# Kernel tuning notes

Hardware: AMD Instinct MI355X
Metric: run time of the kernel (lower is better)

Reference implementation:

```python
import jax, jax.numpy as jnp
import numpy as np
from jax import lax

EPS = 1e-5


def setup_inputs() -> dict:
    key = jax.random.key(0)
    ks = jax.random.split(key, 8)
    B, N, dim = 16, 2048, 128
    x = jax.random.normal(ks[0], (B, 3, N), dtype=jnp.float32)
    W1 = jax.random.normal(ks[1], (dim, 3), dtype=jnp.float32) * 0.1
    W2 = jax.random.normal(ks[2], (dim, dim), dtype=jnp.float32) * 0.05
    W3 = jax.random.normal(ks[3], (dim, dim), dtype=jnp.float32) * 0.05
    zeros = jnp.zeros((dim,), jnp.float32)
    ones = jnp.ones((dim,), jnp.float32)
    return {
        "x": x,
        "W1": W1, "b1": zeros, "g1": ones, "be1": zeros,
        "W2": W2, "b2": zeros, "g2": ones, "be2": zeros,
        "W3": W3, "b3": zeros, "g3": ones, "be3": zeros,
        "k": 8,
    }


def _bn_relu(y, g, be):
    # training-mode batch norm over (B, k, N) per channel, then ReLU
    m = jnp.mean(y, axis=(0, 2, 3), keepdims=True)
    v = jnp.var(y, axis=(0, 2, 3), keepdims=True)
    yhat = (y - m) * lax.rsqrt(v + EPS)
    return jax.nn.relu(yhat * g[None, :, None, None] + be[None, :, None, None])


def _group(x, k):
    # x: [B, 3, N] -> relative kNN offsets [B, 3, k, N] (DGCNN-style, self included)
    sq = jnp.sum(x * x, axis=1)                       # [B, N]
    inner = jnp.einsum('bcn,bcm->bnm', x, x)          # [B, N, N]
    dist = sq[:, :, None] - 2.0 * inner + sq[:, None, :]
    _, idx = lax.top_k(-dist, k)                      # [B, N, k] nearest neighbors
    gathered = jax.vmap(lambda xb, ib: xb[:, ib])(x, idx)  # [B, 3, N, k]
    grouped = gathered - x[:, :, :, None]             # subtract center point
    return jnp.transpose(grouped, (0, 1, 3, 2))       # [B, 3, k, N]


def reference(x, W1, b1, g1, be1, W2, b2, g2, be2, W3, b3, g3, be3, k):
    out = _group(x, k)                                          # [B, 3, k, N]
    h = jnp.einsum('bckn,dc->bdkn', out, W1) + b1[None, :, None, None]
    h = _bn_relu(h, g1, be1)
    h = jnp.einsum('bckn,dc->bdkn', h, W2) + b2[None, :, None, None]
    h = _bn_relu(h, g2, be2)
    h = jnp.einsum('bckn,dc->bdkn', h, W3) + b3[None, :, None, None]
    h = _bn_relu(h, g3, be3)
    return jnp.max(h, axis=2)                                   # [B, dim, N]
```

## Files before the change

### kernel.cpp

```cpp
#include <hip/hip_runtime.h>
#include <hip/hip_bf16.h>
#include <math.h>


#define B_   16
#define N_   2048
#define KNN  8
#define DIM  128
#define P_   (B_*N_*KNN)
#define CAP  128
#define NBLK 2048

typedef __attribute__((ext_vector_type(8))) short bf16x8;
typedef __attribute__((ext_vector_type(4))) short bf16x4;
typedef __attribute__((ext_vector_type(4))) float f32x4;

#define OFF_G     0ull
#define SZ_G      ((size_t)3*P_*4)
#define OFF_Y2B   (OFF_G + SZ_G)
#define SZ_Y2B    ((size_t)DIM*P_*2)
#define OFF_STATS (OFF_Y2B + SZ_Y2B)
#define N_STATS   4112
#define SZ_STATS  ((size_t)N_STATS*8)
#define OFF_AB    (OFF_STATS + SZ_STATS)
#define SZ_AB     4096ull
#define OFF_KPART (OFF_AB + SZ_AB)
#define NKBLK     2048
#define SZ_KPART  ((size_t)9*NKBLK*4)
#define OFF_YMM   (OFF_KPART + SZ_KPART)
#define SZ_YMM    ((size_t)DIM*NBLK*16*4)

#define I_S2   16
#define I_S3   (16 + 8*256)
#define NBANK  8

#define AB_W1F 0
#define AB_A2  512
#define AB_E2  640
#define AB_A3  768
#define AB_E3  896

#define DPP_XOR1   0xB1
#define DPP_XOR2   0x4E
#define DPP_HALFM  0x141
#define DPP_MIRROR 0x140

template<int C>
__device__ __forceinline__ float dppf(float v) {
    return __int_as_float(__builtin_amdgcn_update_dpp(
        __float_as_int(v), __float_as_int(v), C, 0xF, 0xF, false));
}

__device__ __forceinline__ void atomAddD(double* p, double v) {
    __hip_atomic_fetch_add(p, v, __ATOMIC_RELAXED, __HIP_MEMORY_SCOPE_AGENT);
}
__device__ __forceinline__ unsigned short f2bs(float f) {
    const unsigned b = __float_as_uint(f);
    return (unsigned short)((b + 0x7FFFu + ((b >> 16) & 1u)) >> 16);
}
__device__ __forceinline__ float bs2f(unsigned short u) {
    return __uint_as_float(((unsigned)u) << 16);
}

__global__ __launch_bounds__(1024) void knn_group_kernel(
    const float* __restrict__ x, float* __restrict__ g,
    float* __restrict__ kpart, double* __restrict__ st)
{
    __shared__ __align__(16) float4 xs4[N_];
    __shared__ unsigned long long listK[16][CAP];
    __shared__ float spart[16][12];
    const int b   = blockIdx.y;
    const int tid = threadIdx.x;
    const int wv  = tid >> 6;
    const int ln  = tid & 63;
    const int n   = blockIdx.x * 16 + wv;
    const float* xb = x + (size_t)b * 3 * N_;

    if (blockIdx.x == 0 && blockIdx.y == 0)
        for (int i = tid; i < N_STATS; i += 1024) st[i] = 0.0;

    for (int i = tid; i < N_; i += 1024) {
        const float a0 = xb[i], a1 = xb[N_ + i], a2 = xb[2*N_ + i];
        const float sq = __fadd_rn(__fadd_rn(__fmul_rn(a0,a0), __fmul_rn(a1,a1)), __fmul_rn(a2,a2));
        xs4[i] = make_float4(a0, a1, a2, sq);
    }
    __syncthreads();

    const float4 me = xs4[n];
    const float xn0 = me.x, xn1 = me.y, xn2 = me.z, sqn = me.w;

    float dreg[32];
    float lmin = INFINITY;
    #pragma unroll
    for (int i = 0; i < 32; ++i) {
        const float4 q = xs4[ln + 64*i];
        dreg[i] = __fadd_rn(__fmaf_rn(-2.f, __fmaf_rn(xn2, q.z, __fmaf_rn(xn1, q.y, __fmul_rn(xn0, q.x))), sqn), q.w);
        lmin = fminf(lmin, dreg[i]);
    }

    float gm = lmin;
    gm = fminf(gm, __shfl_xor(gm, 1));
    gm = fminf(gm, __shfl_xor(gm, 2));
    gm = fminf(gm, __shfl_xor(gm, 4));
    float Bb = gm;
    Bb = fmaxf(Bb, __shfl_xor(Bb, 8));
    Bb = fmaxf(Bb, __shfl_xor(Bb, 16));
    Bb = fmaxf(Bb, __shfl_xor(Bb, 32));

    unsigned base = 0;
    #pragma unroll
    for (int i = 0; i < 32; ++i) {
        const bool pred = (dreg[i] <= Bb);
        const unsigned long long mk = __ballot(pred);
        if (pred) {
            const unsigned pos = base + (unsigned)__popcll(mk & ((1ull << ln) - 1ull));
            if (pos < CAP) {
                const unsigned u = __float_as_uint(dreg[i]);
                const unsigned od = u ^ ((unsigned)(((int)u) >> 31) | 0x80000000u);
                listK[wv][pos] = (((unsigned long long)od) << 32) | (unsigned)(ln + 64*i);
            }
        }
        base += (unsigned)__popcll(mk);
    }
    const int cnt = (base < CAP) ? (int)base : CAP;

    int myi = 0;
    if (cnt <= 64) {
        unsigned long long K = (ln < cnt) ? listK[wv][ln] : ~0ull;
        #pragma unroll
        for (int k = 2; k <= 64; k <<= 1) {
            #pragma unroll
            for (int j = k >> 1; j >= 1; j >>= 1) {
                const unsigned long long o = __shfl_xor(K, j);
                const bool takeMin = (((ln & j) == 0) == ((ln & k) == 0));
                const bool oLess = (o < K);
                if (takeMin ? oLess : !oLess) K = o;
            }
        }
        myi = (int)(unsigned)K;
    } else {
        unsigned long long K0 = (ln < cnt)      ? listK[wv][ln]      : ~0ull;
        unsigned long long K1 = (ln + 64 < cnt) ? listK[wv][ln + 64] : ~0ull;
        #pragma unroll
        for (int sel = 0; sel < 8; ++sel) {
            unsigned long long p = (K1 < K0) ? K1 : K0;
            #pragma unroll
            for (int m = 1; m < 64; m <<= 1) {
                const unsigned long long o = __shfl_xor(p, m);
                if (o < p) p = o;
            }
            if (ln == sel) myi = (int)(unsigned)p;
            if (K0 == p) K0 = ~0ull;
            if (K1 == p) K1 = ~0ull;
        }
    }

    if (ln < 8) {
        const float4 q = xs4[myi];
        const float g0  = q.x - xn0;
        const float g1v = q.y - xn1;
        const float g2v = q.z - xn2;
        const size_t basep = ((size_t)b*N_ + n) * KNN;
        g[0*P_ + basep + ln] = g0;
        g[1*P_ + basep + ln] = g1v;
        g[2*P_ + basep + ln] = g2v;
        float s0 = g0, s1 = g1v, s2 = g2v;
        float s00 = g0*g0, s01 = g0*g1v, s02 = g0*g2v;
        float s11 = g1v*g1v, s12 = g1v*g2v, s22 = g2v*g2v;
        #pragma unroll
        for (int m = 1; m < 8; m <<= 1) {
            s0 += __shfl_xor(s0, m);  s1 += __shfl_xor(s1, m);  s2 += __shfl_xor(s2, m);
            s00 += __shfl_xor(s00, m); s01 += __shfl_xor(s01, m); s02 += __shfl_xor(s02, m);
            s11 += __shfl_xor(s11, m); s12 += __shfl_xor(s12, m); s22 += __shfl_xor(s22, m);
        }
        if (ln == 0) {
            spart[wv][0] = s0;  spart[wv][1] = s1;  spart[wv][2] = s2;
            spart[wv][3] = s00; spart[wv][4] = s01; spart[wv][5] = s02;
            spart[wv][6] = s11; spart[wv][7] = s12; spart[wv][8] = s22;
        }
    }
    __syncthreads();
    if (tid < 9) {
        float a = 0.f;
        #pragma unroll
        for (int w = 0; w < 16; ++w) a += spart[w][tid];
        kpart[tid*NKBLK + blockIdx.y*128 + blockIdx.x] = a;
    }
}

__global__ __launch_bounds__(1024) void finalize1_kernel(
    const float* __restrict__ kpart, const float* __restrict__ W1,
    const float* __restrict__ b1, const float* __restrict__ g1,
    const float* __restrict__ be1, float* __restrict__ ab)
{
    __shared__ double S9[9];
    const int tid = threadIdx.x;
    const int w = tid >> 6, l = tid & 63;
    if (w < 9) {
        double a = 0.0;
        #pragma unroll
        for (int i = 0; i < 32; ++i) a += (double)kpart[w*NKBLK + l + 64*i];
        #pragma unroll
        for (int m = 1; m < 64; m <<= 1) a += __shfl_xor(a, m);
        if (l == 0) S9[w] = a;
    }
    __syncthreads();
    if (tid < 128) {
        const int d = tid;
        const double inv = 1.0 / (double)P_;
        const double mu0 = S9[0]*inv, mu1 = S9[1]*inv, mu2 = S9[2]*inv;
        const double c00 = S9[3]*inv - mu0*mu0;
        const double c01 = S9[4]*inv - mu0*mu1;
        const double c02 = S9[5]*inv - mu0*mu2;
        const double c11 = S9[6]*inv - mu1*mu1;
        const double c12 = S9[7]*inv - mu1*mu2;
        const double c22 = S9[8]*inv - mu2*mu2;
        const double w0 = W1[d*3+0], w1 = W1[d*3+1], w2 = W1[d*3+2];
        const double mean = w0*mu0 + w1*mu1 + w2*mu2 + (double)b1[d];
        double var = w0*w0*c00 + w1*w1*c11 + w2*w2*c22
                   + 2.0*(w0*w1*c01 + w0*w2*c02 + w1*w2*c12);
        if (var < 0.0) var = 0.0;
        const double r = 1.0 / sqrt(var + 1e-5);
        const double alpha = (double)g1[d] * r;
        const double beta  = (double)be1[d] - mean*alpha;
        ab[AB_W1F + 4*d + 0] = (float)(alpha * w0);
        ab[AB_W1F + 4*d + 1] = (float)(alpha * w1);
        ab[AB_W1F + 4*d + 2] = (float)(alpha * w2);
        ab[AB_W1F + 4*d + 3] = (float)(alpha * (double)b1[d] + beta);
    }
}

__global__ void finalize23_kernel(
    const double* __restrict__ st, int soff,
    const float* __restrict__ gg, const float* __restrict__ bee,
    float* __restrict__ ab, int aoff)
{
    const int d = threadIdx.x;
    if (d >= DIM) return;
    double s1 = 0.0, s2 = 0.0;
    #pragma unroll
    for (int k = 0; k < NBANK; ++k) {
        s1 += st[soff + k*256 + d];
        s2 += st[soff + k*256 + 128 + d];
    }
    const double inv = 1.0 / (double)P_;
    const double mean = s1 * inv;
    double var = s2 * inv - mean*mean;
    if (var < 0.0) var = 0.0;
    const double r = 1.0 / sqrt(var + 1e-5);
    const double alpha = (double)gg[d] * r;
    ab[aoff + d]       = (float)alpha;
    ab[aoff + 128 + d] = (float)((double)bee[d] - mean*alpha);
}

template<int SRC, int MODE>
__global__ __launch_bounds__(512) void conv_kernel(
    const float* __restrict__ gsrc, const unsigned short* __restrict__ ybsrc,
    const float* __restrict__ Wf, const float* __restrict__ ab,
    const float* __restrict__ bias, unsigned short* __restrict__ ybdst,
    unsigned* __restrict__ ymm, double* __restrict__ stats, int statoff)
{
    __shared__ __align__(16) short Hs[128*136];
    const int tid = threadIdx.x;
    const int p0g = blockIdx.x * 128;
    const int w  = tid >> 6;
    const int ln = tid & 63;
    const int lg = ln >> 4, lr = ln & 15;

    bf16x8 afrag[4];
    #pragma unroll
    for (int ks = 0; ks < 4; ++ks) {
        const float* wr = &Wf[(size_t)(16*w + lr)*DIM + (4*ks + lg)*8];
        const float4 a4 = *(const float4*)wr;
        const float4 b4 = *(const float4*)(wr + 4);
        bf16x8 f;
        f[0]=(short)f2bs(a4.x); f[1]=(short)f2bs(a4.y); f[2]=(short)f2bs(a4.z); f[3]=(short)f2bs(a4.w);
        f[4]=(short)f2bs(b4.x); f[5]=(short)f2bs(b4.y); f[6]=(short)f2bs(b4.z); f[7]=(short)f2bs(b4.w);
        afrag[ks] = f;
    }

    if constexpr (SRC == 0) {
        const int sp = tid & 127;
        const int ob = tid >> 7;
        const float gx = gsrc[0*P_ + p0g + sp];
        const float gy = gsrc[1*P_ + p0g + sp];
        const float gz = gsrc[2*P_ + p0g + sp];
        #pragma unroll
        for (int it = 0; it < 4; ++it) {
            const int o = ob + 4*it;
            bf16x8 hv;
            #pragma unroll
            for (int j = 0; j < 8; ++j) {
                const int c = 8*o + j;
                const float4 wf = *(const float4*)&ab[AB_W1F + 4*c];
                const float h = fmaxf(__fmaf_rn(wf.x, gx, __fmaf_rn(wf.y, gy, __fmaf_rn(wf.z, gz, wf.w))), 0.f);
                hv[j] = (short)f2bs(h);
            }
            *(bf16x8*)&Hs[sp*128 + ((o ^ (sp & 7)) * 8)] = hv;
        }
    } else {
        const int myoct = tid & 15;
        const float4 aLo = *(const float4*)&ab[AB_A2 + myoct*8];
        const float4 aHi = *(const float4*)&ab[AB_A2 + myoct*8 + 4];
        const float4 eLo = *(const float4*)&ab[AB_E2 + myoct*8];
        const float4 eHi = *(const float4*)&ab[AB_E2 + myoct*8 + 4];
        const float av[8] = {aLo.x,aLo.y,aLo.z,aLo.w,aHi.x,aHi.y,aHi.z,aHi.w};
        const float ev[8] = {eLo.x,eLo.y,eLo.z,eLo.w,eHi.x,eHi.y,eHi.z,eHi.w};
        #pragma unroll
        for (int it = 0; it < 4; ++it) {
            const int p = it*32 + (tid >> 4);
            const bf16x8 raw = *(const bf16x8*)&ybsrc[(size_t)(p0g + p)*128 + myoct*8];
            bf16x8 hv;
            #pragma unroll
            for (int j = 0; j < 8; ++j) {
                const float v = bs2f((unsigned short)raw[j]);
                hv[j] = (short)f2bs(fmaxf(__fmaf_rn(av[j], v, ev[j]), 0.f));
            }
            *(bf16x8*)&Hs[p*128 + ((myoct ^ (p & 7)) * 8)] = hv;
        }
    }
    __syncthreads();

    f32x4 acc[8];
    #pragma unroll
    for (int j = 0; j < 8; ++j) acc[j] = (f32x4){0.f, 0.f, 0.f, 0.f};

    #pragma unroll
    for (int ks = 0; ks < 4; ++ks) {
        #pragma unroll
        for (int pt = 0; pt < 8; ++pt) {
            const int p = 16*pt + lr;
            const bf16x8 bf = *(const bf16x8*)&Hs[p*128 + (((4*ks + lg) ^ (lr & 7)) * 8)];
            acc[pt] = __builtin_amdgcn_mfma_f32_16x16x32_bf16(afrag[ks], bf, acc[pt], 0, 0, 0);
        }
    }

    const int bank = blockIdx.x & (NBANK-1);
    #pragma unroll
    for (int r = 0; r < 4; ++r) {
        const int d = 16*w + 4*lg + r;
        const float bb = bias[d];
        float v[8];
        #pragma unroll
        for (int pt = 0; pt < 8; ++pt) v[pt] = acc[pt][r] + bb;

        float s1 = ((v[0]+v[1])+(v[2]+v[3])) + ((v[4]+v[5])+(v[6]+v[7]));
        float s2 = ((v[0]*v[0]+v[1]*v[1])+(v[2]*v[2]+v[3]*v[3]))
                 + ((v[4]*v[4]+v[5]*v[5])+(v[6]*v[6]+v[7]*v[7]));
        s1 += dppf<DPP_XOR1>(s1);  s2 += dppf<DPP_XOR1>(s2);
        s1 += dppf<DPP_XOR2>(s1);  s2 += dppf<DPP_XOR2>(s2);
        s1 += dppf<DPP_HALFM>(s1); s2 += dppf<DPP_HALFM>(s2);
        s1 += dppf<DPP_MIRROR>(s1); s2 += dppf<DPP_MIRROR>(s2);
        if (lr == 0) {
            atomAddD(&stats[statoff + bank*256 + d], (double)s1);
            atomAddD(&stats[statoff + bank*256 + 128 + d], (double)s2);
        }

        if constexpr (MODE == 3) {
            #pragma unroll
            for (int pt = 0; pt < 8; ++pt) {
                float mx = v[pt], mn = v[pt];
                mx = fmaxf(mx, dppf<DPP_XOR1>(mx));  mn = fminf(mn, dppf<DPP_XOR1>(mn));
                mx = fmaxf(mx, dppf<DPP_XOR2>(mx));  mn = fminf(mn, dppf<DPP_XOR2>(mn));
                mx = fmaxf(mx, dppf<DPP_HALFM>(mx)); mn = fminf(mn, dppf<DPP_HALFM>(mn));
                if ((lr & 7) == 0) {
                    const int slot = 2*pt + (lr >> 3);
                    ymm[((size_t)d*NBLK + blockIdx.x)*16 + slot] =
                        (unsigned)f2bs(mx) | ((unsigned)f2bs(mn) << 16);
                }
            }
        }
    }

    if constexpr (MODE == 0) {
        __syncthreads();
        const int d0 = 16*w + 4*lg;
        const float4 b4 = *(const float4*)&bias[d0];
        #pragma unroll
        for (int pt = 0; pt < 8; ++pt) {
            const int p = 16*pt + lr;
            bf16x4 pk;
            pk[0] = (short)f2bs(acc[pt][0] + b4.x);
            pk[1] = (short)f2bs(acc[pt][1] + b4.y);
            pk[2] = (short)f2bs(acc[pt][2] + b4.z);
            pk[3] = (short)f2bs(acc[pt][3] + b4.w);
            *(bf16x4*)&Hs[p*136 + d0] = pk;
        }
        __syncthreads();
        #pragma unroll
        for (int it = 0; it < 4; ++it) {
            const int f = it*512 + tid;
            const int row = f >> 4, ch = f & 15;
            const bf16x8 vv = *(const bf16x8*)&Hs[row*136 + ch*8];
            *(bf16x8*)&ybdst[(size_t)(p0g + row)*128 + ch*8] = vv;
        }
    }
}

__global__ __launch_bounds__(256) void bn3max_kernel(
    const unsigned* __restrict__ ymm, const float* __restrict__ ab, float* __restrict__ out)
{
    const int idx = blockIdx.x*256 + threadIdx.x;
    const int n = idx & (N_-1);
    const int d = (idx >> 11) & (DIM-1);
    const int b = idx >> 18;
    const int pt  = b*N_ + n;
    const int blk = pt >> 4;
    const int j   = pt & 15;
    const unsigned pk = ymm[((size_t)d*NBLK + blk)*16 + j];
    const float a = ab[AB_A3 + d], e = ab[AB_E3 + d];
    const float mx = bs2f((unsigned short)(pk & 0xFFFF));
    const float mn = bs2f((unsigned short)(pk >> 16));
    const float v = (a >= 0.f) ? mx : mn;
    out[idx] = fmaxf(__fmaf_rn(a, v, e), 0.f);
}

extern "C" void kernel_launch(void* const* d_in, const int* in_sizes, int n_in,
                              void* d_out, int out_size, void* d_ws, size_t ws_size,
                              hipStream_t stream) {
    (void)in_sizes; (void)n_in; (void)out_size; (void)ws_size;
    const float* x   = (const float*)d_in[0];
    const float* W1  = (const float*)d_in[1];
    const float* b1  = (const float*)d_in[2];
    const float* g1  = (const float*)d_in[3];
    const float* be1 = (const float*)d_in[4];
    const float* W2  = (const float*)d_in[5];
    const float* b2  = (const float*)d_in[6];
    const float* g2  = (const float*)d_in[7];
    const float* be2 = (const float*)d_in[8];
    const float* W3  = (const float*)d_in[9];
    const float* b3  = (const float*)d_in[10];
    const float* g3  = (const float*)d_in[11];
    const float* be3 = (const float*)d_in[12];

    float*  out = (float*)d_out;
    char*   ws  = (char*)d_ws;
    float*          g   = (float*)(ws + OFF_G);
    unsigned short* y2t = (unsigned short*)(ws + OFF_Y2B);
    double*         st  = (double*)(ws + OFF_STATS);
    float*          ab  = (float*)(ws + OFF_AB);
    float*          kp  = (float*)(ws + OFF_KPART);
    unsigned*       ymm = (unsigned*)(ws + OFF_YMM);

    knn_group_kernel<<<dim3(128, B_), 1024, 0, stream>>>(x, g, kp, st);
    finalize1_kernel<<<1, 1024, 0, stream>>>(kp, W1, b1, g1, be1, ab);
    conv_kernel<0,0><<<NBLK, 512, 0, stream>>>(g, nullptr, W2, ab, b2, y2t, nullptr, st, I_S2);
    finalize23_kernel<<<1, 128, 0, stream>>>(st, I_S2, g2, be2, ab, AB_A2);
    conv_kernel<1,3><<<NBLK, 512, 0, stream>>>(nullptr, y2t, W3, ab, b3, nullptr, ymm, st, I_S3);
    finalize23_kernel<<<1, 128, 0, stream>>>(st, I_S3, g3, be3, ab, AB_A3);
    bn3max_kernel<<<(B_*DIM*N_)/256, 256, 0, stream>>>(ymm, ab, out);
}
```

Before: 153.5 us.

## Fold BN finalize kernels into consumers and process two points per kNN wave

Removes the two single-block finalize23 launches by having each conv_kernel<1,3> block and each bn3max block recompute the per-channel BN affine from the double stats into shared memory. Also makes each kNN wave handle two query points, halving the grid and reusing each shared-memory point load for two distance rows. This trades two launches and their serial gaps for redundant stats reads in every block (many blocks in bn3max), and doubles distance registers per thread in the kNN kernel, which may lower occupancy.

```diff
diff --git a/kernel.cpp b/kernel.cpp
--- a/kernel.cpp
+++ b/kernel.cpp
@@ -10,6 +10,7 @@
 #define P_   (B_*N_*KNN)
 #define CAP  128
 #define NBLK 2048
+#define KBLKS 1024
 
 typedef __attribute__((ext_vector_type(8))) short bf16x8;
 typedef __attribute__((ext_vector_type(4))) short bf16x4;
@@ -25,8 +26,7 @@
 #define OFF_AB    (OFF_STATS + SZ_STATS)
 #define SZ_AB     4096ull
 #define OFF_KPART (OFF_AB + SZ_AB)
-#define NKBLK     2048
-#define SZ_KPART  ((size_t)9*NKBLK*4)
+#define SZ_KPART  ((size_t)9*2048*4)
 #define OFF_YMM   (OFF_KPART + SZ_KPART)
 #define SZ_YMM    ((size_t)DIM*NBLK*16*4)
 
@@ -35,10 +35,6 @@
 #define NBANK  8
 
 #define AB_W1F 0
-#define AB_A2  512
-#define AB_E2  640
-#define AB_A3  768
-#define AB_E3  896
 
 #define DPP_XOR1   0xB1
 #define DPP_XOR2   0x4E
@@ -62,42 +58,10 @@
     return __uint_as_float(((unsigned)u) << 16);
 }
 
-__global__ __launch_bounds__(1024) void knn_group_kernel(
-    const float* __restrict__ x, float* __restrict__ g,
-    float* __restrict__ kpart, double* __restrict__ st)
-{
-    __shared__ __align__(16) float4 xs4[N_];
-    __shared__ unsigned long long listK[16][CAP];
-    __shared__ float spart[16][12];
-    const int b   = blockIdx.y;
-    const int tid = threadIdx.x;
-    const int wv  = tid >> 6;
-    const int ln  = tid & 63;
-    const int n   = blockIdx.x * 16 + wv;
-    const float* xb = x + (size_t)b * 3 * N_;
-
-    if (blockIdx.x == 0 && blockIdx.y == 0)
-        for (int i = tid; i < N_STATS; i += 1024) st[i] = 0.0;
-
-    for (int i = tid; i < N_; i += 1024) {
-        const float a0 = xb[i], a1 = xb[N_ + i], a2 = xb[2*N_ + i];
-        const float sq = __fadd_rn(__fadd_rn(__fmul_rn(a0,a0), __fmul_rn(a1,a1)), __fmul_rn(a2,a2));
-        xs4[i] = make_float4(a0, a1, a2, sq);
-    }
-    __syncthreads();
-
-    const float4 me = xs4[n];
-    const float xn0 = me.x, xn1 = me.y, xn2 = me.z, sqn = me.w;
-
-    float dreg[32];
-    float lmin = INFINITY;
-    #pragma unroll
-    for (int i = 0; i < 32; ++i) {
-        const float4 q = xs4[ln + 64*i];
-        dreg[i] = __fadd_rn(__fmaf_rn(-2.f, __fmaf_rn(xn2, q.z, __fmaf_rn(xn1, q.y, __fmul_rn(xn0, q.x))), sqn), q.w);
-        lmin = fminf(lmin, dreg[i]);
-    }
-
+__device__ __forceinline__ int select8(
+    const float (&dreg)[32], float lmin,
+    unsigned long long* __restrict__ listKw, int ln)
+{
     float gm = lmin;
     gm = fminf(gm, __shfl_xor(gm, 1));
     gm = fminf(gm, __shfl_xor(gm, 2));
@@ -117,7 +81,7 @@
             if (pos < CAP) {
                 const unsigned u = __float_as_uint(dreg[i]);
                 const unsigned od = u ^ ((unsigned)(((int)u) >> 31) | 0x80000000u);
-                listK[wv][pos] = (((unsigned long long)od) << 32) | (unsigned)(ln + 64*i);
+                listKw[pos] = (((unsigned long long)od) << 32) | (unsigned)(ln + 64*i);
             }
         }
         base += (unsigned)__popcll(mk);
@@ -126,7 +90,7 @@
 
     int myi = 0;
     if (cnt <= 64) {
-        unsigned long long K = (ln < cnt) ? listK[wv][ln] : ~0ull;
+        unsigned long long K = (ln < cnt) ? listKw[ln] : ~0ull;
         #pragma unroll
         for (int k = 2; k <= 64; k <<= 1) {
             #pragma unroll
@@ -139,8 +103,8 @@
         }
         myi = (int)(unsigned)K;
     } else {
-        unsigned long long K0 = (ln < cnt)      ? listK[wv][ln]      : ~0ull;
-        unsigned long long K1 = (ln + 64 < cnt) ? listK[wv][ln + 64] : ~0ull;
+        unsigned long long K0 = (ln < cnt)      ? listKw[ln]      : ~0ull;
+        unsigned long long K1 = (ln + 64 < cnt) ? listKw[ln + 64] : ~0ull;
         #pragma unroll
         for (int sel = 0; sel < 8; ++sel) {
             unsigned long long p = (K1 < K0) ? K1 : K0;
@@ -154,19 +118,88 @@
             if (K1 == p) K1 = ~0ull;
         }
     }
+    return myi;
+}
+
+__global__ __launch_bounds__(1024) void knn_group_kernel(
+    const float* __restrict__ x, float* __restrict__ g,
+    float* __restrict__ kpart, double* __restrict__ st)
+{
+    __shared__ __align__(16) float4 xs4[N_];
+    __shared__ unsigned long long listK[16][CAP];
+    __shared__ float spart[16][12];
+    const int b   = blockIdx.y;
+    const int tid = threadIdx.x;
+    const int wv  = tid >> 6;
+    const int ln  = tid & 63;
+    const int nA  = blockIdx.x * 32 + 2*wv;
+    const int nB  = nA + 1;
+    const float* xb = x + (size_t)b * 3 * N_;
+
+    if (blockIdx.x == 0 && blockIdx.y == 0)
+        for (int i = tid; i < N_STATS; i += 1024) st[i] = 0.0;
+
+    for (int i = tid; i < N_; i += 1024) {
+        const float a0 = xb[i], a1 = xb[N_ + i], a2 = xb[2*N_ + i];
+        const float sq = __fadd_rn(__fadd_rn(__fmul_rn(a0,a0), __fmul_rn(a1,a1)), __fmul_rn(a2,a2));
+        xs4[i] = make_float4(a0, a1, a2, sq);
+    }
+    __syncthreads();
+
+    const float4 meA = xs4[nA];
+    const float4 meB = xs4[nB];
+
+    float dA[32], dB[32];
+    float lminA = INFINITY, lminB = INFINITY;
+    #pragma unroll
+    for (int i = 0; i < 32; ++i) {
+        const float4 q = xs4[ln + 64*i];
+        dA[i] = __fadd_rn(__fmaf_rn(-2.f,
+                    __fmaf_rn(meA.z, q.z, __fmaf_rn(meA.y, q.y, __fmul_rn(meA.x, q.x))),
+                    meA.w), q.w);
+        dB[i] = __fadd_rn(__fmaf_rn(-2.f,
+                    __fmaf_rn(meB.z, q.z, __fmaf_rn(meB.y, q.y, __fmul_rn(meB.x, q.x))),
+                    meB.w), q.w);
+        lminA = fminf(lminA, dA[i]);
+        lminB = fminf(lminB, dB[i]);
+    }
+
+    float s0=0.f,s1=0.f,s2=0.f,s00=0.f,s01=0.f,s02=0.f,s11=0.f,s12=0.f,s22=0.f;
+
+    {
+        const int myi = select8(dA, lminA, listK[wv], ln);
+        if (ln < 8) {
+            const float4 q = xs4[myi];
+            const float g0  = q.x - meA.x;
+            const float g1v = q.y - meA.y;
+            const float g2v = q.z - meA.z;
+            const size_t basep = ((size_t)b*N_ + nA) * KNN;
+            g[0*P_ + basep + ln] = g0;
+            g[1*P_ + basep + ln] = g1v;
+            g[2*P_ + basep + ln] = g2v;
+            s0 += g0; s1 += g1v; s2 += g2v;
+            s00 = fmaf(g0,g0,s00); s01 = fmaf(g0,g1v,s01); s02 = fmaf(g0,g2v,s02);
+            s11 = fmaf(g1v,g1v,s11); s12 = fmaf(g1v,g2v,s12); s22 = fmaf(g2v,g2v,s22);
+        }
+    }
+    {
+        const int myi = select8(dB, lminB, listK[wv], ln);
+        if (ln < 8) {
+            const float4 q = xs4[myi];
+            const float g0  = q.x - meB.x;
+            const float g1v = q.y - meB.y;
+            const float g2v = q.z - meB.z;
+            const size_t basep = ((size_t)b*N_ + nB) * KNN;
+            g[0*P_ + basep + ln] = g0;
+            g[1*P_ + basep + ln] = g1v;
+            g[2*P_ + basep + ln] = g2v;
+            s0 += g0; s1 += g1v; s2 += g2v;
+            s00 = fmaf(g0,g0,s00); s01 = fmaf(g0,g1v,s01); s02 = fmaf(g0,g2v,s02);
+            s11 = fmaf(g1v,g1v,s11); s12 = fmaf(g1v,g2v,s12); s22 = fmaf(g2v,g2v,s22);
+        }
+    }
 
     if (ln < 8) {
-        const float4 q = xs4[myi];
-        const float g0  = q.x - xn0;
-        const float g1v = q.y - xn1;
-        const float g2v = q.z - xn2;
-        const size_t basep = ((size_t)b*N_ + n) * KNN;
-        g[0*P_ + basep + ln] = g0;
-        g[1*P_ + basep + ln] = g1v;
-        g[2*P_ + basep + ln] = g2v;
-        float s0 = g0, s1 = g1v, s2 = g2v;
-        float s00 = g0*g0, s01 = g0*g1v, s02 = g0*g2v;
-        float s11 = g1v*g1v, s12 = g1v*g2v, s22 = g2v*g2v;
         #pragma unroll
         for (int m = 1; m < 8; m <<= 1) {
             s0 += __shfl_xor(s0, m);  s1 += __shfl_xor(s1, m);  s2 += __shfl_xor(s2, m);
@@ -184,7 +217,7 @@
         float a = 0.f;
         #pragma unroll
         for (int w = 0; w < 16; ++w) a += spart[w][tid];
-        kpart[tid*NKBLK + blockIdx.y*128 + blockIdx.x] = a;
+        kpart[tid*KBLKS + blockIdx.y*64 + blockIdx.x] = a;
     }
 }
 
@@ -199,7 +232,7 @@
     if (w < 9) {
         double a = 0.0;
         #pragma unroll
-        for (int i = 0; i < 32; ++i) a += (double)kpart[w*NKBLK + l + 64*i];
+        for (int i = 0; i < 16; ++i) a += (double)kpart[w*KBLKS + l + 64*i];
         #pragma unroll
         for (int m = 1; m < 64; m <<= 1) a += __shfl_xor(a, m);
         if (l == 0) S9[w] = a;
@@ -230,13 +263,11 @@
     }
 }
 
-__global__ void finalize23_kernel(
-    const double* __restrict__ st, int soff,
+__device__ __forceinline__ void bn_affine_block(
+    const double* __restrict__ st, int soff, int d,
     const float* __restrict__ gg, const float* __restrict__ bee,
-    float* __restrict__ ab, int aoff)
-{
-    const int d = threadIdx.x;
-    if (d >= DIM) return;
+    float* __restrict__ al, float* __restrict__ el)
+{
     double s1 = 0.0, s2 = 0.0;
     #pragma unroll
     for (int k = 0; k < NBANK; ++k) {
@@ -249,8 +280,8 @@
     if (var < 0.0) var = 0.0;
     const double r = 1.0 / sqrt(var + 1e-5);
     const double alpha = (double)gg[d] * r;
-    ab[aoff + d]       = (float)alpha;
-    ab[aoff + 128 + d] = (float)((double)bee[d] - mean*alpha);
+    al[d] = (float)alpha;
+    el[d] = (float)((double)bee[d] - mean*alpha);
 }
 
 template<int SRC, int MODE>
@@ -258,14 +289,21 @@
     const float* __restrict__ gsrc, const unsigned short* __restrict__ ybsrc,
     const float* __restrict__ Wf, const float* __restrict__ ab,
     const float* __restrict__ bias, unsigned short* __restrict__ ybdst,
-    unsigned* __restrict__ ymm, double* __restrict__ stats, int statoff)
+    unsigned* __restrict__ ymm, double* __restrict__ stats, int statoff,
+    const float* __restrict__ gprev, const float* __restrict__ beprev)
 {
     __shared__ __align__(16) short Hs[128*136];
+    __shared__ float a2l[DIM], e2l[DIM];
     const int tid = threadIdx.x;
     const int p0g = blockIdx.x * 128;
     const int w  = tid >> 6;
     const int ln = tid & 63;
     const int lg = ln >> 4, lr = ln & 15;
+
+    if constexpr (SRC == 1) {
+        if (tid < DIM) bn_affine_block(stats, I_S2, tid, gprev, beprev, a2l, e2l);
+        __syncthreads();
+    }
 
     bf16x8 afrag[4];
     #pragma unroll
@@ -300,10 +338,10 @@
         }
     } else {
         const int myoct = tid & 15;
-        const float4 aLo = *(const float4*)&ab[AB_A2 + myoct*8];
-        const float4 aHi = *(const float4*)&ab[AB_A2 + myoct*8 + 4];
-        const float4 eLo = *(const float4*)&ab[AB_E2 + myoct*8];
-        const float4 eHi = *(const float4*)&ab[AB_E2 + myoct*8 + 4];
+        const float4 aLo = *(const float4*)&a2l[myoct*8];
+        const float4 aHi = *(const float4*)&a2l[myoct*8 + 4];
+        const float4 eLo = *(const float4*)&e2l[myoct*8];
+        const float4 eHi = *(const float4*)&e2l[myoct*8 + 4];
         const float av[8] = {aLo.x,aLo.y,aLo.z,aLo.w,aHi.x,aHi.y,aHi.z,aHi.w};
         const float ev[8] = {eLo.x,eLo.y,eLo.z,eLo.w,eHi.x,eHi.y,eHi.z,eHi.w};
         #pragma unroll
@@ -398,9 +436,16 @@
 }
 
 __global__ __launch_bounds__(256) void bn3max_kernel(
-    const unsigned* __restrict__ ymm, const float* __restrict__ ab, float* __restrict__ out)
-{
-    const int idx = blockIdx.x*256 + threadIdx.x;
+    const unsigned* __restrict__ ymm, const double* __restrict__ stats,
+    const float* __restrict__ g3, const float* __restrict__ be3,
+    float* __restrict__ out)
+{
+    __shared__ float a3l[DIM], e3l[DIM];
+    const int tid = threadIdx.x;
+    if (tid < DIM) bn_affine_block(stats, I_S3, tid, g3, be3, a3l, e3l);
+    __syncthreads();
+
+    const int idx = blockIdx.x*256 + tid;
     const int n = idx & (N_-1);
     const int d = (idx >> 11) & (DIM-1);
     const int b = idx >> 18;
@@ -408,7 +453,7 @@
     const int blk = pt >> 4;
     const int j   = pt & 15;
     const unsigned pk = ymm[((size_t)d*NBLK + blk)*16 + j];
-    const float a = ab[AB_A3 + d], e = ab[AB_E3 + d];
+    const float a = a3l[d], e = e3l[d];
     const float mx = bs2f((unsigned short)(pk & 0xFFFF));
     const float mn = bs2f((unsigned short)(pk >> 16));
     const float v = (a >= 0.f) ? mx : mn;
@@ -442,11 +487,9 @@
     float*          kp  = (float*)(ws + OFF_KPART);
     unsigned*       ymm = (unsigned*)(ws + OFF_YMM);
 
-    knn_group_kernel<<<dim3(128, B_), 1024, 0, stream>>>(x, g, kp, st);
+    knn_group_kernel<<<dim3(N_/32, B_), 1024, 0, stream>>>(x, g, kp, st);
     finalize1_kernel<<<1, 1024, 0, stream>>>(kp, W1, b1, g1, be1, ab);
-    conv_kernel<0,0><<<NBLK, 512, 0, stream>>>(g, nullptr, W2, ab, b2, y2t, nullptr, st, I_S2);
-    finalize23_kernel<<<1, 128, 0, stream>>>(st, I_S2, g2, be2, ab, AB_A2);
-    conv_kernel<1,3><<<NBLK, 512, 0, stream>>>(nullptr, y2t, W3, ab, b3, nullptr, ymm, st, I_S3);
-    finalize23_kernel<<<1, 128, 0, stream>>>(st, I_S3, g3, be3, ab, AB_A3);
-    bn3max_kernel<<<(B_*DIM*N_)/256, 256, 0, stream>>>(ymm, ab, out);
-}
+    conv_kernel<0,0><<<NBLK, 512, 0, stream>>>(g, nullptr, W2, ab, b2, y2t, nullptr, st, I_S2, nullptr, nullptr);
+    conv_kernel<1,3><<<NBLK, 512, 0, stream>>>(nullptr, y2t, W3, ab, b3, nullptr, ymm, st, I_S3, g2, be2);
+    bn3max_kernel<<<(B_*DIM*N_)/256, 256, 0, stream>>>(ymm, st, g3, be3, out);
+}
```

After: 228.9 us. 1.49x slower.
